# Kernel tuning notes

Hardware: AMD Instinct MI355X
Metric: run time of the kernel (lower is better)

Reference implementation:

```python
import jax, jax.numpy as jnp
import numpy as np

L_LEVELS = 10
LEVEL_DIM = 4
BASE_RES = 16
T_HASH = 2 ** 21
DEG_VIEW = 4
DENSITY_BIAS = -1.0
RGB_PADDING = 0.001
RES = (BASE_RES * 2 ** np.arange(L_LEVELS)).astype(np.float32)  # 16..8192
CORNERS = np.array([[(i >> 2) & 1, (i >> 1) & 1, i & 1] for i in range(8)], np.int32)  # [8,3]
P1 = jnp.uint32(2654435761)
P2 = jnp.uint32(805459861)


def hash_grid_encode(pts, embeddings):
    """pts [N,3] in [-1,1]; embeddings [L,T,D] -> [N,L,D] trilinear hash-grid features."""
    x01 = (pts + 1.0) * 0.5  # [N,3] in [0,1]

    def level(emb, r):
        pos = x01 * r - 0.5  # align_corners=False style
        p0 = jnp.floor(pos)
        frac = pos - p0  # [N,3]
        coords = (p0.astype(jnp.int32)[:, None, :] + CORNERS).astype(jnp.uint32)  # [N,8,3]
        h = coords[..., 0] ^ (coords[..., 1] * P1) ^ (coords[..., 2] * P2)
        idx = (h & jnp.uint32(T_HASH - 1)).astype(jnp.int32)  # [N,8]
        w = jnp.prod(jnp.where(CORNERS == 1, frac[:, None, :], 1.0 - frac[:, None, :]), axis=-1)  # [N,8]
        vals = emb[idx]  # [N,8,D]
        return jnp.einsum('ncd,nc->nd', vals, w)

    feats = jax.vmap(level)(embeddings, jnp.asarray(RES))  # [L,N,D]
    return jnp.moveaxis(feats, 0, 1)  # [N,L,D]


def pos_enc(d, min_deg=0, max_deg=DEG_VIEW):
    scales = 2.0 ** jnp.arange(min_deg, max_deg, dtype=jnp.float32)
    xb = (d[..., None, :] * scales[:, None]).reshape(*d.shape[:-1], -1)  # [...,3*deg]
    four = jnp.sin(jnp.concatenate([xb, xb + 0.5 * jnp.pi], axis=-1))
    return jnp.concatenate([d, four], axis=-1)  # [..., 3 + 6*deg] = 27


def setup_inputs() -> dict:
    key = jax.random.key(0)
    ks = jax.random.split(key, 10)
    B, S, n = 1024, 32, 6
    means = jax.random.uniform(ks[0], (B, S, n, 3), minval=-1.0, maxval=1.0)
    stds = jax.random.uniform(ks[1], (B, S, n), minval=0.001, maxval=0.05)
    vd = jax.random.normal(ks[2], (B, 3))
    viewdirs = vd / jnp.linalg.norm(vd, axis=-1, keepdims=True)
    embeddings = jax.random.normal(ks[3], (L_LEVELS, T_HASH, LEVEL_DIM)) * 0.1

    def lin(k, i, o):
        return jax.random.normal(k, (i, o)) * (1.0 / np.sqrt(i))

    return {
        'rand': 0,
        'means': means, 'stds': stds, 'viewdirs': viewdirs, 'embeddings': embeddings,
        'Wd0': lin(ks[4], 40, 64), 'bd0': jnp.zeros(64),
        'Wd1': lin(ks[5], 64, 256), 'bd1': jnp.zeros(256),
        'Wv0': lin(ks[6], 283, 256), 'bv0': jnp.zeros(256),
        'Wv1': lin(ks[7], 539, 256), 'bv1': jnp.zeros(256),
        'Wr': lin(ks[8], 256, 3), 'br': jnp.zeros(3),
    }


def reference(rand, means, stds, viewdirs, embeddings, Wd0, bd0, Wd1, bd1,
              Wv0, bv0, Wv1, bv1, Wr, br):
    B, S, n = means.shape[:3]
    # --- predict_density ---
    feats = hash_grid_encode(means.reshape(-1, 3), embeddings)
    feats = feats.reshape(B, S, n, L_LEVELS, LEVEL_DIM)
    gs = jnp.asarray(RES)
    # erf re-weighting by per-level grid size (ZipNeRF anti-aliasing)
    w = jax.lax.erf(1.0 / jnp.clip(jnp.sqrt(8.0 * stds[..., None] ** 2 * gs ** 2), 1e-10))  # [B,S,n,L]
    feat = (feats * w[..., None]).mean(axis=-3).reshape(B, S, L_LEVELS * LEVEL_DIM)  # mean over multisamples n
    h = jax.nn.relu(feat @ Wd0 + bd0)
    x = h @ Wd1 + bd1  # [B,S,256] bottleneck
    density = jax.nn.softplus(x[..., 0] + DENSITY_BIAS)
    # --- view-dependent rgb branch ---
    dir_enc = pos_enc(viewdirs)  # [B,27]
    de = jnp.broadcast_to(dir_enc[:, None, :], (B, S, dir_enc.shape[-1]))
    x_in = jnp.concatenate([x, de], axis=-1)  # [B,S,283]
    h = jax.nn.relu(x_in @ Wv0 + bv0)
    h = jnp.concatenate([h, x_in], axis=-1)  # skip connection at layer 0 -> [B,S,539]
    h = jax.nn.relu(h @ Wv1 + bv1)
    rgb = jax.nn.sigmoid(h @ Wr + br)  # rgb_premultiplier=1, rgb_bias=0
    rgb = rgb * (1.0 + 2.0 * RGB_PADDING) - RGB_PADDING
    return density, rgb
```

## Files before the change

### kernel.cpp

```cpp
#include <hip/hip_runtime.h>

#define HASH_T    2097152u
#define HASH_MASK 2097151u
#define PRIME1 2654435761u
#define PRIME2 805459861u

typedef __attribute__((ext_vector_type(8))) short bf16x8;
typedef __attribute__((ext_vector_type(4))) float f32x4;
typedef __attribute__((ext_vector_type(4))) unsigned short us4;

#define LDS_STRIDE 328

__device__ __forceinline__ unsigned short bf16_hi(float x){
    unsigned u = __float_as_uint(x);
    return (unsigned short)((u + 0x7FFFu + ((u >> 16) & 1u)) >> 16);
}
__device__ __forceinline__ float bf16f(unsigned short h){
    return __uint_as_float((unsigned)h << 16);
}
__device__ __forceinline__ void split2(float x, unsigned short& h, unsigned short& l){
    h = bf16_hi(x);
    l = bf16_hi(x - bf16f(h));
}

__global__ __launch_bounds__(256) void pack_weights_kernel(
    const float* __restrict__ Wd0, const float* __restrict__ Wd1,
    const float* __restrict__ Wv0, const float* __restrict__ Wv1,
    unsigned short* __restrict__ pk)
{
    int tid = blockIdx.x * 256 + threadIdx.x;
    if (tid >= 424 * 512) return;
    int pair = tid >> 9;
    int li   = tid & 511;
    int lane = li >> 3, j = li & 7;
    int kq = ((lane >> 4) << 3) + j;
    int cl = lane & 15;
    float w;
    if (pair < 8) {
        int idx = pair; int kt = idx >> 2, ct = idx & 3;
        int k = kt * 32 + kq, c = ct * 16 + cl;
        w = (k < 40) ? Wd0[k * 64 + c] : 0.0f;
    } else if (pair < 40) {
        int idx = pair - 8; int kt = idx >> 4, ct = idx & 15;
        int k = kt * 32 + kq, c = ct * 16 + cl;
        w = Wd1[k * 256 + c];
    } else if (pair < 168) {
        int idx = pair - 40; int kt = idx >> 4, ct = idx & 15;
        int k = kt * 32 + kq, c = ct * 16 + cl;
        w = Wv0[k * 256 + c];
    } else {
        int idx = pair - 168;
        int kt = idx >> 4, ct = idx & 15;
        int k = kt * 32 + kq, c = ct * 16 + cl;
        int refr = (k < 256) ? (k + 256) : (k - 256);
        w = Wv1[refr * 256 + c];
    }
    unsigned short h, l; split2(w, h, l);
    pk[(size_t)pair * 1024 + li]       = h;
    pk[(size_t)pair * 1024 + 512 + li] = l;
}

template<int KT, int NC>
__device__ __forceinline__ void gemm32(
    const unsigned short* __restrict__ pkBase, int NCT, int ct0, int kOff,
    const unsigned short (*Ahi)[LDS_STRIDE], const unsigned short (*Alo)[LDS_STRIDE],
    int lane, f32x4 acc[NC][2])
{
    const int r = lane & 15;
    const int kg = (lane >> 4) * 8;
    bf16x8 ah[NC], al[NC];
    #pragma unroll
    for (int ci = 0; ci < NC; ++ci) {
        const unsigned short* pf = pkBase + (size_t)(ct0 + ci) * 1024 + (size_t)lane * 8;
        ah[ci] = *reinterpret_cast<const bf16x8*>(pf);
        al[ci] = *reinterpret_cast<const bf16x8*>(pf + 512);
    }
    #pragma unroll
    for (int kt = 0; kt < KT; ++kt) {
        bf16x8 ahn[NC], aln[NC];
        if (kt + 1 < KT) {
            #pragma unroll
            for (int ci = 0; ci < NC; ++ci) {
                const unsigned short* pf = pkBase
                    + (size_t)((kt + 1) * NCT + ct0 + ci) * 1024 + (size_t)lane * 8;
                ahn[ci] = *reinterpret_cast<const bf16x8*>(pf);
                aln[ci] = *reinterpret_cast<const bf16x8*>(pf + 512);
            }
        }
        const int ke = kOff + kt * 32 + kg;
        bf16x8 bh[2], bl[2];
        #pragma unroll
        for (int st = 0; st < 2; ++st) {
            bh[st] = *reinterpret_cast<const bf16x8*>(&Ahi[st * 16 + r][ke]);
            bl[st] = *reinterpret_cast<const bf16x8*>(&Alo[st * 16 + r][ke]);
        }
        #pragma unroll
        for (int ci = 0; ci < NC; ++ci) {
            #pragma unroll
            for (int st = 0; st < 2; ++st) {
                acc[ci][st] = __builtin_amdgcn_mfma_f32_16x16x32_bf16(ah[ci], bh[st], acc[ci][st], 0, 0, 0);
                acc[ci][st] = __builtin_amdgcn_mfma_f32_16x16x32_bf16(ah[ci], bl[st], acc[ci][st], 0, 0, 0);
                acc[ci][st] = __builtin_amdgcn_mfma_f32_16x16x32_bf16(al[ci], bh[st], acc[ci][st], 0, 0, 0);
            }
        }
        if (kt + 1 < KT) {
            #pragma unroll
            for (int ci = 0; ci < NC; ++ci) { ah[ci] = ahn[ci]; al[ci] = aln[ci]; }
        }
    }
}

template<int NC, bool RELU>
__device__ __forceinline__ void epi32(
    f32x4 acc[NC][2], int ct0, int lane, const float* bias, int outOff,
    unsigned short (*Ahi)[LDS_STRIDE], unsigned short (*Alo)[LDS_STRIDE])
{
    const int r = lane & 15, g = lane >> 4;
    #pragma unroll
    for (int ci = 0; ci < NC; ++ci) {
        const int c0 = (ct0 + ci) * 16 + g * 4;
        const float4 bb = *reinterpret_cast<const float4*>(&bias[c0]);
        #pragma unroll
        for (int st = 0; st < 2; ++st) {
            const int s = st * 16 + r;
            float v[4] = { acc[ci][st][0] + bb.x, acc[ci][st][1] + bb.y,
                           acc[ci][st][2] + bb.z, acc[ci][st][3] + bb.w };
            us4 H, L;
            #pragma unroll
            for (int q = 0; q < 4; ++q) {
                float vv = RELU ? fmaxf(v[q], 0.0f) : v[q];
                unsigned short h, l; split2(vv, h, l);
                H[q] = h; L[q] = l;
            }
            *reinterpret_cast<us4*>(&Ahi[s][outOff + c0]) = H;
            *reinterpret_cast<us4*>(&Alo[s][outOff + c0]) = L;
        }
    }
}

__global__ __launch_bounds__(256, 3) void zip_fused_kernel(
    const float* __restrict__ means, const float* __restrict__ stds,
    const float* __restrict__ vdirs, const float* __restrict__ emb,
    const unsigned short* __restrict__ pk,
    const float* __restrict__ bd0, const float* __restrict__ bd1,
    const float* __restrict__ Wv0, const float* __restrict__ bv0,
    const float* __restrict__ Wv1, const float* __restrict__ bv1,
    const float* __restrict__ Wr,  const float* __restrict__ br,
    float* __restrict__ outD, float* __restrict__ outRGB)
{
    __shared__ __align__(16) unsigned short sAhi[32][LDS_STRIDE];
    __shared__ __align__(16) unsigned short sAlo[32][LDS_STRIDE];
    __shared__ float sDe[32];
    __shared__ float sDv0[256];
    __shared__ float sDv1[256];

    const int t = threadIdx.x;
    const int lane = t & 63;
    const int w = t >> 6;
    const int b = blockIdx.x;
    const int base = b * 32;

    if (t < 192) {
        int s = t / 6, j = t - s * 6;
        us4 z = {0, 0, 0, 0};
        *reinterpret_cast<us4*>(&sAhi[s][40 + j * 4]) = z;
        *reinterpret_cast<us4*>(&sAlo[s][40 + j * 4]) = z;
    }
    if (t < 27) {
        float d0 = vdirs[b * 3 + 0], d1 = vdirs[b * 3 + 1], d2 = vdirs[b * 3 + 2];
        float val;
        if (t < 3) val = (t == 0) ? d0 : ((t == 1) ? d1 : d2);
        else {
            int u = t - 3, half = u / 12, jk = u % 12;
            int j = jk / 3, k = jk % 3;
            float dk = (k == 0) ? d0 : ((k == 1) ? d1 : d2);
            float xb = dk * (float)(1 << j);
            val = sinf(half ? (xb + 1.57079632679489662f) : xb);
        }
        sDe[t] = val;
    }
    __syncthreads();

    {
        const int s = t >> 3, n = t & 7;
        const bool act = (n < 6);
        float mx = 0.f, my = 0.f, mz = 0.f, sd2_8 = 0.f;
        if (act) {
            const float* mp = means + ((size_t)(base + s) * 6 + n) * 3;
            mx = mp[0]; my = mp[1]; mz = mp[2];
            float sd = stds[(size_t)(base + s) * 6 + n];
            sd2_8 = 8.0f * sd * sd;
        }
        const float inv6 = 1.0f / 6.0f;
        #pragma unroll 2
        for (int l = 0; l < 10; ++l) {
            float r = (float)(16 << l);
            float a0 = 0.f, a1 = 0.f, a2 = 0.f, a3 = 0.f;
            if (act) {
                float px = (mx + 1.0f) * 0.5f * r - 0.5f;
                float py = (my + 1.0f) * 0.5f * r - 0.5f;
                float pz = (mz + 1.0f) * 0.5f * r - 0.5f;
                float fx = floorf(px), fy = floorf(py), fz = floorf(pz);
                float rx = px - fx, ry = py - fy, rz = pz - fz;
                int ix = (int)fx, iy = (int)fy, iz = (int)fz;
                unsigned hx[2] = { (unsigned)ix,          (unsigned)(ix + 1) };
                unsigned hy[2] = { (unsigned)iy * PRIME1, (unsigned)(iy + 1) * PRIME1 };
                unsigned hz[2] = { (unsigned)iz * PRIME2, (unsigned)(iz + 1) * PRIME2 };
                float wx[2] = { 1.0f - rx, rx };
                float wy[2] = { 1.0f - ry, ry };
                float wz[2] = { 1.0f - rz, rz };
                float wl = erff(1.0f / fmaxf(sqrtf(sd2_8 * r * r), 1e-10f));
                #pragma unroll
                for (int c = 0; c < 8; ++c) {
                    int cx = (c >> 2) & 1, cy = (c >> 1) & 1, cz = c & 1;
                    unsigned idx = (hx[cx] ^ hy[cy] ^ hz[cz]) & HASH_MASK;
                    const float4 e = *reinterpret_cast<const float4*>(
                        emb + ((size_t)l * HASH_T + idx) * 4u);
                    float wgt = wx[cx] * wy[cy] * wz[cz];
                    a0 += wgt * e.x; a1 += wgt * e.y; a2 += wgt * e.z; a3 += wgt * e.w;
                }
                a0 *= wl; a1 *= wl; a2 *= wl; a3 *= wl;
            }
            #pragma unroll
            for (int m = 1; m < 8; m <<= 1) {
                a0 += __shfl_xor(a0, m);
                a1 += __shfl_xor(a1, m);
                a2 += __shfl_xor(a2, m);
                a3 += __shfl_xor(a3, m);
            }
            if (n == 0) {
                float o[4] = { a0 * inv6, a1 * inv6, a2 * inv6, a3 * inv6 };
                us4 H, L;
                #pragma unroll
                for (int q = 0; q < 4; ++q) {
                    unsigned short h, lo; split2(o[q], h, lo);
                    H[q] = h; L[q] = lo;
                }
                *reinterpret_cast<us4*>(&sAhi[s][l * 4]) = H;
                *reinterpret_cast<us4*>(&sAlo[s][l * 4]) = L;
            }
        }
    }
    __syncthreads();

    {
        int c = t;
        float a0 = bv0[c], a1 = bv1[c];
        #pragma unroll 3
        for (int k = 0; k < 27; ++k) {
            float dv = sDe[k];
            a0 += dv * Wv0[(256 + k) * 256 + c];
            a1 += dv * Wv1[(512 + k) * 256 + c];
        }
        sDv0[c] = a0; sDv1[c] = a1;
    }
    __syncthreads();

    {
        f32x4 acc[1][2] = {};
        gemm32<2, 1>(pk, 4, w, 0, sAhi, sAlo, lane, acc);
        __syncthreads();
        epi32<1, true>(acc, w, lane, bd0, 0, sAhi, sAlo);
    }
    __syncthreads();

    {
        f32x4 acc[4][2] = {};
        gemm32<2, 4>(pk + 8192, 16, w * 4, 0, sAhi, sAlo, lane, acc);
        if (w == 0 && (lane >> 4) == 0) {
            #pragma unroll
            for (int st = 0; st < 2; ++st) {
                float x0 = acc[0][st][0] + bd1[0];
                int s = st * 16 + (lane & 15);
                float vv = x0 - 1.0f;
                outD[base + s] = fmaxf(vv, 0.0f) + log1pf(expf(-fabsf(vv)));
            }
        }
        __syncthreads();
        epi32<4, false>(acc, w * 4, lane, bd1, 64, sAhi, sAlo);
    }
    __syncthreads();

    f32x4 px[4][2] = {};
    gemm32<8, 4>(pk + 172032, 16, w * 4, 64, sAhi, sAlo, lane, px);
    __syncthreads();

    {
        f32x4 acc[4][2] = {};
        gemm32<8, 4>(pk + 40960, 16, w * 4, 64, sAhi, sAlo, lane, acc);
        __syncthreads();
        epi32<4, true>(acc, w * 4, lane, sDv0, 64, sAhi, sAlo);
    }
    __syncthreads();

    {
        gemm32<8, 4>(pk + 303104, 16, w * 4, 64, sAhi, sAlo, lane, px);
        __syncthreads();
        epi32<4, true>(px, w * 4, lane, sDv1, 64, sAhi, sAlo);
    }
    __syncthreads();

    {
        int s = t >> 3, j = t & 7, k0 = 64 + j * 32;
        float p0 = 0.f, p1 = 0.f, p2 = 0.f;
        #pragma unroll 2
        for (int q = 0; q < 4; ++q) {
            us4 vh[2], vl[2];
            *reinterpret_cast<uint4*>(vh) = *reinterpret_cast<const uint4*>(&sAhi[s][k0 + q * 8]);
            *reinterpret_cast<uint4*>(vl) = *reinterpret_cast<const uint4*>(&sAlo[s][k0 + q * 8]);
            #pragma unroll
            for (int e = 0; e < 8; ++e) {
                int k = j * 32 + q * 8 + e;
                float hv = bf16f(((const unsigned short*)vh)[e]) + bf16f(((const unsigned short*)vl)[e]);
                p0 += hv * Wr[k * 3 + 0];
                p1 += hv * Wr[k * 3 + 1];
                p2 += hv * Wr[k * 3 + 2];
            }
        }
        #pragma unroll
        for (int m = 1; m < 8; m <<= 1) {
            p0 += __shfl_xor(p0, m);
            p1 += __shfl_xor(p1, m);
            p2 += __shfl_xor(p2, m);
        }
        if (j < 3) {
            float a = ((j == 0) ? p0 : (j == 1) ? p1 : p2) + br[j];
            float sg = 1.0f / (1.0f + expf(-a));
            outRGB[(size_t)(base + s) * 3 + j] = sg * 1.002f - 0.001f;
        }
    }
}

extern "C" void kernel_launch(void* const* d_in, const int* in_sizes, int n_in,
                              void* d_out, int out_size, void* d_ws, size_t ws_size,
                              hipStream_t stream) {
    const float* means = (const float*)d_in[1];
    const float* stds_ = (const float*)d_in[2];
    const float* vdirs = (const float*)d_in[3];
    const float* emb   = (const float*)d_in[4];
    const float* Wd0 = (const float*)d_in[5];
    const float* bd0 = (const float*)d_in[6];
    const float* Wd1 = (const float*)d_in[7];
    const float* bd1 = (const float*)d_in[8];
    const float* Wv0 = (const float*)d_in[9];
    const float* bv0 = (const float*)d_in[10];
    const float* Wv1 = (const float*)d_in[11];
    const float* bv1 = (const float*)d_in[12];
    const float* Wr  = (const float*)d_in[13];
    const float* br  = (const float*)d_in[14];

    const int B  = in_sizes[3] / 3;
    const int NS = B * 32;

    unsigned short* pk = (unsigned short*)d_ws;

    hipLaunchKernelGGL(pack_weights_kernel, dim3((424 * 512 + 255) / 256), dim3(256), 0, stream,
                       Wd0, Wd1, Wv0, Wv1, pk);

    float* outD   = (float*)d_out;
    float* outRGB = outD + NS;
    hipLaunchKernelGGL(zip_fused_kernel, dim3(B), dim3(256), 0, stream,
                       means, stds_, vdirs, emb, pk,
                       bd0, bd1, Wv0, bv0, Wv1, bv1, Wr, br,
                       outD, outRGB);
}
```

Measured before the change: 191.4 us.

## Keep density-branch activations in single bf16 and shrink LDS to raise occupancy

The hash-grid features and the first density hidden layer are now stored as plain bf16 in a separate 32x64 LDS buffer, not as hi/lo bf16 pairs. The two density GEMMs use a new two-MFMA routine that drops the low-activation term. The bottleneck and view-branch activations keep hi/lo in smaller 264-wide buffers, which cuts LDS per block, and launch bounds are raised from 3 to 4 blocks per CU. The trade is lower precision in the density MLP inputs and some register pressure from the new bound.

After: 216.4 us. +13.1%, slower.

```diff
diff --git a/kernel.cpp b/kernel.cpp
--- a/kernel.cpp
+++ b/kernel.cpp
@@ -9,7 +9,7 @@
 typedef __attribute__((ext_vector_type(4))) float f32x4;
 typedef __attribute__((ext_vector_type(4))) unsigned short us4;
 
-#define LDS_STRIDE 328
+#define XS 264
 
 __device__ __forceinline__ unsigned short bf16_hi(float x){
     unsigned u = __float_as_uint(x);
@@ -62,8 +62,8 @@
 
 template<int KT, int NC>
 __device__ __forceinline__ void gemm32(
-    const unsigned short* __restrict__ pkBase, int NCT, int ct0, int kOff,
-    const unsigned short (*Ahi)[LDS_STRIDE], const unsigned short (*Alo)[LDS_STRIDE],
+    const unsigned short* __restrict__ pkBase, int NCT, int ct0,
+    const unsigned short (*Bhi)[XS], const unsigned short (*Blo)[XS],
     int lane, f32x4 acc[NC][2])
 {
     const int r = lane & 15;
@@ -87,12 +87,12 @@
                 aln[ci] = *reinterpret_cast<const bf16x8*>(pf + 512);
             }
         }
-        const int ke = kOff + kt * 32 + kg;
+        const int ke = kt * 32 + kg;
         bf16x8 bh[2], bl[2];
         #pragma unroll
         for (int st = 0; st < 2; ++st) {
-            bh[st] = *reinterpret_cast<const bf16x8*>(&Ahi[st * 16 + r][ke]);
-            bl[st] = *reinterpret_cast<const bf16x8*>(&Alo[st * 16 + r][ke]);
+            bh[st] = *reinterpret_cast<const bf16x8*>(&Bhi[st * 16 + r][ke]);
+            bl[st] = *reinterpret_cast<const bf16x8*>(&Blo[st * 16 + r][ke]);
         }
         #pragma unroll
         for (int ci = 0; ci < NC; ++ci) {
@@ -110,10 +110,56 @@
     }
 }
 
+template<int KT, int NC>
+__device__ __forceinline__ void gemm_sf(
+    const unsigned short* __restrict__ pkBase, int NCT, int ct0,
+    const unsigned short (*B)[64], int lane, f32x4 acc[NC][2])
+{
+    const int r = lane & 15;
+    const int kg = (lane >> 4) * 8;
+    bf16x8 ah[NC], al[NC];
+    #pragma unroll
+    for (int ci = 0; ci < NC; ++ci) {
+        const unsigned short* pf = pkBase + (size_t)(ct0 + ci) * 1024 + (size_t)lane * 8;
+        ah[ci] = *reinterpret_cast<const bf16x8*>(pf);
+        al[ci] = *reinterpret_cast<const bf16x8*>(pf + 512);
+    }
+    #pragma unroll
+    for (int kt = 0; kt < KT; ++kt) {
+        bf16x8 ahn[NC], aln[NC];
+        if (kt + 1 < KT) {
+            #pragma unroll
+            for (int ci = 0; ci < NC; ++ci) {
+                const unsigned short* pf = pkBase
+                    + (size_t)((kt + 1) * NCT + ct0 + ci) * 1024 + (size_t)lane * 8;
+                ahn[ci] = *reinterpret_cast<const bf16x8*>(pf);
+                aln[ci] = *reinterpret_cast<const bf16x8*>(pf + 512);
+            }
+        }
+        const int ke = kt * 32 + kg;
+        bf16x8 bh[2];
+        #pragma unroll
+        for (int st = 0; st < 2; ++st)
+            bh[st] = *reinterpret_cast<const bf16x8*>(&B[st * 16 + r][ke]);
+        #pragma unroll
+        for (int ci = 0; ci < NC; ++ci) {
+            #pragma unroll
+            for (int st = 0; st < 2; ++st) {
+                acc[ci][st] = __builtin_amdgcn_mfma_f32_16x16x32_bf16(ah[ci], bh[st], acc[ci][st], 0, 0, 0);
+                acc[ci][st] = __builtin_amdgcn_mfma_f32_16x16x32_bf16(al[ci], bh[st], acc[ci][st], 0, 0, 0);
+            }
+        }
+        if (kt + 1 < KT) {
+            #pragma unroll
+            for (int ci = 0; ci < NC; ++ci) { ah[ci] = ahn[ci]; al[ci] = aln[ci]; }
+        }
+    }
+}
+
 template<int NC, bool RELU>
 __device__ __forceinline__ void epi32(
-    f32x4 acc[NC][2], int ct0, int lane, const float* bias, int outOff,
-    unsigned short (*Ahi)[LDS_STRIDE], unsigned short (*Alo)[LDS_STRIDE])
+    f32x4 acc[NC][2], int ct0, int lane, const float* bias,
+    unsigned short (*Bhi)[XS], unsigned short (*Blo)[XS])
 {
     const int r = lane & 15, g = lane >> 4;
     #pragma unroll
@@ -132,13 +178,13 @@
                 unsigned short h, l; split2(vv, h, l);
                 H[q] = h; L[q] = l;
             }
-            *reinterpret_cast<us4*>(&Ahi[s][outOff + c0]) = H;
-            *reinterpret_cast<us4*>(&Alo[s][outOff + c0]) = L;
-        }
-    }
-}
-
-__global__ __launch_bounds__(256, 3) void zip_fused_kernel(
+            *reinterpret_cast<us4*>(&Bhi[s][c0]) = H;
+            *reinterpret_cast<us4*>(&Blo[s][c0]) = L;
+        }
+    }
+}
+
+__global__ __launch_bounds__(256, 4) void zip_fused_kernel(
     const float* __restrict__ means, const float* __restrict__ stds,
     const float* __restrict__ vdirs, const float* __restrict__ emb,
     const unsigned short* __restrict__ pk,
@@ -148,8 +194,9 @@
     const float* __restrict__ Wr,  const float* __restrict__ br,
     float* __restrict__ outD, float* __restrict__ outRGB)
 {
-    __shared__ __align__(16) unsigned short sAhi[32][LDS_STRIDE];
-    __shared__ __align__(16) unsigned short sAlo[32][LDS_STRIDE];
+    __shared__ __align__(16) unsigned short sF[32][64];
+    __shared__ __align__(16) unsigned short sXhi[32][XS];
+    __shared__ __align__(16) unsigned short sXlo[32][XS];
     __shared__ float sDe[32];
     __shared__ float sDv0[256];
     __shared__ float sDv1[256];
@@ -163,8 +210,7 @@
     if (t < 192) {
         int s = t / 6, j = t - s * 6;
         us4 z = {0, 0, 0, 0};
-        *reinterpret_cast<us4*>(&sAhi[s][40 + j * 4]) = z;
-        *reinterpret_cast<us4*>(&sAlo[s][40 + j * 4]) = z;
+        *reinterpret_cast<us4*>(&sF[s][40 + j * 4]) = z;
     }
     if (t < 27) {
         float d0 = vdirs[b * 3 + 0], d1 = vdirs[b * 3 + 1], d2 = vdirs[b * 3 + 2];
@@ -229,15 +275,12 @@
                 a3 += __shfl_xor(a3, m);
             }
             if (n == 0) {
-                float o[4] = { a0 * inv6, a1 * inv6, a2 * inv6, a3 * inv6 };
-                us4 H, L;
-                #pragma unroll
-                for (int q = 0; q < 4; ++q) {
-                    unsigned short h, lo; split2(o[q], h, lo);
-                    H[q] = h; L[q] = lo;
-                }
-                *reinterpret_cast<us4*>(&sAhi[s][l * 4]) = H;
-                *reinterpret_cast<us4*>(&sAlo[s][l * 4]) = L;
+                us4 H;
+                H[0] = bf16_hi(a0 * inv6);
+                H[1] = bf16_hi(a1 * inv6);
+                H[2] = bf16_hi(a2 * inv6);
+                H[3] = bf16_hi(a3 * inv6);
+                *reinterpret_cast<us4*>(&sF[s][l * 4]) = H;
             }
         }
     }
@@ -258,15 +301,27 @@
 
     {
         f32x4 acc[1][2] = {};
-        gemm32<2, 1>(pk, 4, w, 0, sAhi, sAlo, lane, acc);
+        gemm_sf<2, 1>(pk, 4, w, sF, lane, acc);
         __syncthreads();
-        epi32<1, true>(acc, w, lane, bd0, 0, sAhi, sAlo);
+        const int r = lane & 15, g = lane >> 4;
+        const int c0 = w * 16 + g * 4;
+        const float4 bb = *reinterpret_cast<const float4*>(&bd0[c0]);
+        #pragma unroll
+        for (int st = 0; st < 2; ++st) {
+            const int s = st * 16 + r;
+            us4 H;
+            H[0] = bf16_hi(fmaxf(acc[0][st][0] + bb.x, 0.0f));
+            H[1] = bf16_hi(fmaxf(acc[0][st][1] + bb.y, 0.0f));
+            H[2] = bf16_hi(fmaxf(acc[0][st][2] + bb.z, 0.0f));
+            H[3] = bf16_hi(fmaxf(acc[0][st][3] + bb.w, 0.0f));
+            *reinterpret_cast<us4*>(&sF[s][c0]) = H;
+        }
     }
     __syncthreads();
 
     {
         f32x4 acc[4][2] = {};
-        gemm32<2, 4>(pk + 8192, 16, w * 4, 0, sAhi, sAlo, lane, acc);
+        gemm_sf<2, 4>(pk + 8192, 16, w * 4, sF, lane, acc);
         if (w == 0 && (lane >> 4) == 0) {
             #pragma unroll
             for (int st = 0; st < 2; ++st) {
@@ -276,41 +331,40 @@
                 outD[base + s] = fmaxf(vv, 0.0f) + log1pf(expf(-fabsf(vv)));
             }
         }
+        epi32<4, false>(acc, w * 4, lane, bd1, sXhi, sXlo);
+    }
+    __syncthreads();
+
+    f32x4 px[4][2] = {};
+    gemm32<8, 4>(pk + 172032, 16, w * 4, sXhi, sXlo, lane, px);
+    __syncthreads();
+
+    {
+        f32x4 acc[4][2] = {};
+        gemm32<8, 4>(pk + 40960, 16, w * 4, sXhi, sXlo, lane, acc);
         __syncthreads();
-        epi32<4, false>(acc, w * 4, lane, bd1, 64, sAhi, sAlo);
-    }
-    __syncthreads();
-
-    f32x4 px[4][2] = {};
-    gemm32<8, 4>(pk + 172032, 16, w * 4, 64, sAhi, sAlo, lane, px);
-    __syncthreads();
-
-    {
-        f32x4 acc[4][2] = {};
-        gemm32<8, 4>(pk + 40960, 16, w * 4, 64, sAhi, sAlo, lane, acc);
+        epi32<4, true>(acc, w * 4, lane, sDv0, sXhi, sXlo);
+    }
+    __syncthreads();
+
+    {
+        gemm32<8, 4>(pk + 303104, 16, w * 4, sXhi, sXlo, lane, px);
         __syncthreads();
-        epi32<4, true>(acc, w * 4, lane, sDv0, 64, sAhi, sAlo);
-    }
-    __syncthreads();
-
-    {
-        gemm32<8, 4>(pk + 303104, 16, w * 4, 64, sAhi, sAlo, lane, px);
-        __syncthreads();
-        epi32<4, true>(px, w * 4, lane, sDv1, 64, sAhi, sAlo);
-    }
-    __syncthreads();
-
-    {
-        int s = t >> 3, j = t & 7, k0 = 64 + j * 32;
+        epi32<4, true>(px, w * 4, lane, sDv1, sXhi, sXlo);
+    }
+    __syncthreads();
+
+    {
+        int s = t >> 3, j = t & 7, k0 = j * 32;
         float p0 = 0.f, p1 = 0.f, p2 = 0.f;
         #pragma unroll 2
         for (int q = 0; q < 4; ++q) {
             us4 vh[2], vl[2];
-            *reinterpret_cast<uint4*>(vh) = *reinterpret_cast<const uint4*>(&sAhi[s][k0 + q * 8]);
-            *reinterpret_cast<uint4*>(vl) = *reinterpret_cast<const uint4*>(&sAlo[s][k0 + q * 8]);
+            *reinterpret_cast<uint4*>(vh) = *reinterpret_cast<const uint4*>(&sXhi[s][k0 + q * 8]);
+            *reinterpret_cast<uint4*>(vl) = *reinterpret_cast<const uint4*>(&sXlo[s][k0 + q * 8]);
             #pragma unroll
             for (int e = 0; e < 8; ++e) {
-                int k = j * 32 + q * 8 + e;
+                int k = k0 + q * 8 + e;
                 float hv = bf16f(((const unsigned short*)vh)[e]) + bf16f(((const unsigned short*)vl)[e]);
                 p0 += hv * Wr[k * 3 + 0];
                 p1 += hv * Wr[k * 3 + 1];
```

## Halve samples per block and spread hash-grid corners across threads

Applied to the files above, without the earlier changes.

Each block now handles 16 samples instead of 32, which doubles the grid size and halves LDS use per block. The MFMA GEMMs shrink to a single 16-row tile. The hash-grid encode changes its thread mapping: each thread owns one corner for three multisamples instead of all eight corners for one sample. It processes two levels per iteration to issue more independent gathers, then reduces across 16 lanes. The aim is more memory-level parallelism and occupancy for the random embedding gathers, at the cost of loading the weight fragments twice as often per sample and recomputing the view-direction encoding per block.

After: 189.4 us. No clear change (-1.1%).

```diff
diff --git a/kernel.cpp b/kernel.cpp
--- a/kernel.cpp
+++ b/kernel.cpp
@@ -61,10 +61,10 @@
 }
 
 template<int KT, int NC>
-__device__ __forceinline__ void gemm32(
+__device__ __forceinline__ void gemm16(
     const unsigned short* __restrict__ pkBase, int NCT, int ct0, int kOff,
     const unsigned short (*Ahi)[LDS_STRIDE], const unsigned short (*Alo)[LDS_STRIDE],
-    int lane, f32x4 acc[NC][2])
+    int lane, f32x4 acc[NC])
 {
     const int r = lane & 15;
     const int kg = (lane >> 4) * 8;
@@ -88,20 +88,13 @@
             }
         }
         const int ke = kOff + kt * 32 + kg;
-        bf16x8 bh[2], bl[2];
-        #pragma unroll
-        for (int st = 0; st < 2; ++st) {
-            bh[st] = *reinterpret_cast<const bf16x8*>(&Ahi[st * 16 + r][ke]);
-            bl[st] = *reinterpret_cast<const bf16x8*>(&Alo[st * 16 + r][ke]);
-        }
+        bf16x8 bh = *reinterpret_cast<const bf16x8*>(&Ahi[r][ke]);
+        bf16x8 bl = *reinterpret_cast<const bf16x8*>(&Alo[r][ke]);
         #pragma unroll
         for (int ci = 0; ci < NC; ++ci) {
-            #pragma unroll
-            for (int st = 0; st < 2; ++st) {
-                acc[ci][st] = __builtin_amdgcn_mfma_f32_16x16x32_bf16(ah[ci], bh[st], acc[ci][st], 0, 0, 0);
-                acc[ci][st] = __builtin_amdgcn_mfma_f32_16x16x32_bf16(ah[ci], bl[st], acc[ci][st], 0, 0, 0);
-                acc[ci][st] = __builtin_amdgcn_mfma_f32_16x16x32_bf16(al[ci], bh[st], acc[ci][st], 0, 0, 0);
-            }
+            acc[ci] = __builtin_amdgcn_mfma_f32_16x16x32_bf16(ah[ci], bh, acc[ci], 0, 0, 0);
+            acc[ci] = __builtin_amdgcn_mfma_f32_16x16x32_bf16(ah[ci], bl, acc[ci], 0, 0, 0);
+            acc[ci] = __builtin_amdgcn_mfma_f32_16x16x32_bf16(al[ci], bh, acc[ci], 0, 0, 0);
         }
         if (kt + 1 < KT) {
             #pragma unroll
@@ -111,8 +104,8 @@
 }
 
 template<int NC, bool RELU>
-__device__ __forceinline__ void epi32(
-    f32x4 acc[NC][2], int ct0, int lane, const float* bias, int outOff,
+__device__ __forceinline__ void epi16(
+    f32x4 acc[NC], int ct0, int lane, const float* bias, int outOff,
     unsigned short (*Ahi)[LDS_STRIDE], unsigned short (*Alo)[LDS_STRIDE])
 {
     const int r = lane & 15, g = lane >> 4;
@@ -120,21 +113,17 @@
     for (int ci = 0; ci < NC; ++ci) {
         const int c0 = (ct0 + ci) * 16 + g * 4;
         const float4 bb = *reinterpret_cast<const float4*>(&bias[c0]);
+        float v[4] = { acc[ci][0] + bb.x, acc[ci][1] + bb.y,
+                       acc[ci][2] + bb.z, acc[ci][3] + bb.w };
+        us4 H, L;
         #pragma unroll
-        for (int st = 0; st < 2; ++st) {
-            const int s = st * 16 + r;
-            float v[4] = { acc[ci][st][0] + bb.x, acc[ci][st][1] + bb.y,
-                           acc[ci][st][2] + bb.z, acc[ci][st][3] + bb.w };
-            us4 H, L;
-            #pragma unroll
-            for (int q = 0; q < 4; ++q) {
-                float vv = RELU ? fmaxf(v[q], 0.0f) : v[q];
-                unsigned short h, l; split2(vv, h, l);
-                H[q] = h; L[q] = l;
-            }
-            *reinterpret_cast<us4*>(&Ahi[s][outOff + c0]) = H;
-            *reinterpret_cast<us4*>(&Alo[s][outOff + c0]) = L;
-        }
+        for (int q = 0; q < 4; ++q) {
+            float vv = RELU ? fmaxf(v[q], 0.0f) : v[q];
+            unsigned short h, l; split2(vv, h, l);
+            H[q] = h; L[q] = l;
+        }
+        *reinterpret_cast<us4*>(&Ahi[r][outOff + c0]) = H;
+        *reinterpret_cast<us4*>(&Alo[r][outOff + c0]) = L;
     }
 }
 
@@ -148,8 +137,8 @@
     const float* __restrict__ Wr,  const float* __restrict__ br,
     float* __restrict__ outD, float* __restrict__ outRGB)
 {
-    __shared__ __align__(16) unsigned short sAhi[32][LDS_STRIDE];
-    __shared__ __align__(16) unsigned short sAlo[32][LDS_STRIDE];
+    __shared__ __align__(16) unsigned short sAhi[16][LDS_STRIDE];
+    __shared__ __align__(16) unsigned short sAlo[16][LDS_STRIDE];
     __shared__ float sDe[32];
     __shared__ float sDv0[256];
     __shared__ float sDv1[256];
@@ -158,16 +147,17 @@
     const int lane = t & 63;
     const int w = t >> 6;
     const int b = blockIdx.x;
-    const int base = b * 32;
-
-    if (t < 192) {
+    const int ray = b >> 1;
+    const int base = b * 16;
+
+    if (t < 96) {
         int s = t / 6, j = t - s * 6;
         us4 z = {0, 0, 0, 0};
         *reinterpret_cast<us4*>(&sAhi[s][40 + j * 4]) = z;
         *reinterpret_cast<us4*>(&sAlo[s][40 + j * 4]) = z;
     }
     if (t < 27) {
-        float d0 = vdirs[b * 3 + 0], d1 = vdirs[b * 3 + 1], d2 = vdirs[b * 3 + 2];
+        float d0 = vdirs[ray * 3 + 0], d1 = vdirs[ray * 3 + 1], d2 = vdirs[ray * 3 + 2];
         float val;
         if (t < 3) val = (t == 0) ? d0 : ((t == 1) ? d1 : d2);
         else {
@@ -182,62 +172,72 @@
     __syncthreads();
 
     {
-        const int s = t >> 3, n = t & 7;
-        const bool act = (n < 6);
-        float mx = 0.f, my = 0.f, mz = 0.f, sd2_8 = 0.f;
-        if (act) {
+        const int s = t >> 4, u = t & 15;
+        const int c = u >> 1, h = u & 1;
+        const int cxb = (c >> 2) & 1, cyb = (c >> 1) & 1, czb = c & 1;
+        float mx[3], my[3], mz[3], s28[3];
+        #pragma unroll
+        for (int q = 0; q < 3; ++q) {
+            int n = h * 3 + q;
             const float* mp = means + ((size_t)(base + s) * 6 + n) * 3;
-            mx = mp[0]; my = mp[1]; mz = mp[2];
+            mx[q] = mp[0]; my[q] = mp[1]; mz[q] = mp[2];
             float sd = stds[(size_t)(base + s) * 6 + n];
-            sd2_8 = 8.0f * sd * sd;
+            s28[q] = 8.0f * sd * sd;
         }
         const float inv6 = 1.0f / 6.0f;
-        #pragma unroll 2
-        for (int l = 0; l < 10; ++l) {
-            float r = (float)(16 << l);
-            float a0 = 0.f, a1 = 0.f, a2 = 0.f, a3 = 0.f;
-            if (act) {
-                float px = (mx + 1.0f) * 0.5f * r - 0.5f;
-                float py = (my + 1.0f) * 0.5f * r - 0.5f;
-                float pz = (mz + 1.0f) * 0.5f * r - 0.5f;
-                float fx = floorf(px), fy = floorf(py), fz = floorf(pz);
-                float rx = px - fx, ry = py - fy, rz = pz - fz;
-                int ix = (int)fx, iy = (int)fy, iz = (int)fz;
-                unsigned hx[2] = { (unsigned)ix,          (unsigned)(ix + 1) };
-                unsigned hy[2] = { (unsigned)iy * PRIME1, (unsigned)(iy + 1) * PRIME1 };
-                unsigned hz[2] = { (unsigned)iz * PRIME2, (unsigned)(iz + 1) * PRIME2 };
-                float wx[2] = { 1.0f - rx, rx };
-                float wy[2] = { 1.0f - ry, ry };
-                float wz[2] = { 1.0f - rz, rz };
-                float wl = erff(1.0f / fmaxf(sqrtf(sd2_8 * r * r), 1e-10f));
+        #pragma unroll 1
+        for (int lp = 0; lp < 5; ++lp) {
+            float4 ev[2][3];
+            float cw[2][3];
+            #pragma unroll
+            for (int dl = 0; dl < 2; ++dl) {
+                const int l = lp * 2 + dl;
+                const float r = (float)(16 << l);
+                const float* embL = emb + (size_t)l * HASH_T * 4u;
                 #pragma unroll
-                for (int c = 0; c < 8; ++c) {
-                    int cx = (c >> 2) & 1, cy = (c >> 1) & 1, cz = c & 1;
-                    unsigned idx = (hx[cx] ^ hy[cy] ^ hz[cz]) & HASH_MASK;
-                    const float4 e = *reinterpret_cast<const float4*>(
-                        emb + ((size_t)l * HASH_T + idx) * 4u);
-                    float wgt = wx[cx] * wy[cy] * wz[cz];
-                    a0 += wgt * e.x; a1 += wgt * e.y; a2 += wgt * e.z; a3 += wgt * e.w;
+                for (int q = 0; q < 3; ++q) {
+                    float px = (mx[q] + 1.0f) * 0.5f * r - 0.5f;
+                    float py = (my[q] + 1.0f) * 0.5f * r - 0.5f;
+                    float pz = (mz[q] + 1.0f) * 0.5f * r - 0.5f;
+                    float fx = floorf(px), fy = floorf(py), fz = floorf(pz);
+                    float rx = px - fx, ry = py - fy, rz = pz - fz;
+                    unsigned hx = (unsigned)((int)fx + cxb);
+                    unsigned hy = (unsigned)((int)fy + cyb) * PRIME1;
+                    unsigned hz = (unsigned)((int)fz + czb) * PRIME2;
+                    unsigned idx = (hx ^ hy ^ hz) & HASH_MASK;
+                    float wx = cxb ? rx : 1.0f - rx;
+                    float wy = cyb ? ry : 1.0f - ry;
+                    float wz = czb ? rz : 1.0f - rz;
+                    float wl = erff(1.0f / fmaxf(sqrtf(s28[q] * r * r), 1e-10f));
+                    cw[dl][q] = wx * wy * wz * wl;
+                    ev[dl][q] = *reinterpret_cast<const float4*>(embL + (size_t)idx * 4u);
                 }
-                a0 *= wl; a1 *= wl; a2 *= wl; a3 *= wl;
             }
             #pragma unroll
-            for (int m = 1; m < 8; m <<= 1) {
-                a0 += __shfl_xor(a0, m);
-                a1 += __shfl_xor(a1, m);
-                a2 += __shfl_xor(a2, m);
-                a3 += __shfl_xor(a3, m);
-            }
-            if (n == 0) {
-                float o[4] = { a0 * inv6, a1 * inv6, a2 * inv6, a3 * inv6 };
-                us4 H, L;
+            for (int dl = 0; dl < 2; ++dl) {
+                float a0 = cw[dl][0]*ev[dl][0].x + cw[dl][1]*ev[dl][1].x + cw[dl][2]*ev[dl][2].x;
+                float a1 = cw[dl][0]*ev[dl][0].y + cw[dl][1]*ev[dl][1].y + cw[dl][2]*ev[dl][2].y;
+                float a2 = cw[dl][0]*ev[dl][0].z + cw[dl][1]*ev[dl][1].z + cw[dl][2]*ev[dl][2].z;
+                float a3 = cw[dl][0]*ev[dl][0].w + cw[dl][1]*ev[dl][1].w + cw[dl][2]*ev[dl][2].w;
                 #pragma unroll
-                for (int q = 0; q < 4; ++q) {
-                    unsigned short h, lo; split2(o[q], h, lo);
-                    H[q] = h; L[q] = lo;
+                for (int m = 1; m < 16; m <<= 1) {
+                    a0 += __shfl_xor(a0, m);
+                    a1 += __shfl_xor(a1, m);
+                    a2 += __shfl_xor(a2, m);
+                    a3 += __shfl_xor(a3, m);
                 }
-                *reinterpret_cast<us4*>(&sAhi[s][l * 4]) = H;
-                *reinterpret_cast<us4*>(&sAlo[s][l * 4]) = L;
+                if (u == 0) {
+                    const int l = lp * 2 + dl;
+                    float o[4] = { a0 * inv6, a1 * inv6, a2 * inv6, a3 * inv6 };
+                    us4 H, L;
+                    #pragma unroll
+                    for (int q = 0; q < 4; ++q) {
+                        unsigned short hh, ll; split2(o[q], hh, ll);
+                        H[q] = hh; L[q] = ll;
+                    }
+                    *reinterpret_cast<us4*>(&sAhi[s][l * 4]) = H;
+                    *reinterpret_cast<us4*>(&sAlo[s][l * 4]) = L;
+                }
             }
         }
     }
@@ -257,50 +257,46 @@
     __syncthreads();
 
     {
-        f32x4 acc[1][2] = {};
-        gemm32<2, 1>(pk, 4, w, 0, sAhi, sAlo, lane, acc);
+        f32x4 acc[1] = {};
+        gemm16<2, 1>(pk, 4, w, 0, sAhi, sAlo, lane, acc);
         __syncthreads();
-        epi32<1, true>(acc, w, lane, bd0, 0, sAhi, sAlo);
-    }
-    __syncthreads();
-
-    {
-        f32x4 acc[4][2] = {};
-        gemm32<2, 4>(pk + 8192, 16, w * 4, 0, sAhi, sAlo, lane, acc);
-        if (w == 0 && (lane >> 4) == 0) {
-            #pragma unroll
-            for (int st = 0; st < 2; ++st) {
-                float x0 = acc[0][st][0] + bd1[0];
-                int s = st * 16 + (lane & 15);
-                float vv = x0 - 1.0f;
-                outD[base + s] = fmaxf(vv, 0.0f) + log1pf(expf(-fabsf(vv)));
-            }
+        epi16<1, true>(acc, w, lane, bd0, 0, sAhi, sAlo);
+    }
+    __syncthreads();
+
+    {
+        f32x4 acc[4] = {};
+        gemm16<2, 4>(pk + 8192, 16, w * 4, 0, sAhi, sAlo, lane, acc);
+        if (w == 0 && lane < 16) {
+            float x0 = acc[0][0] + bd1[0];
+            float vv = x0 - 1.0f;
+            outD[base + lane] = fmaxf(vv, 0.0f) + log1pf(expf(-fabsf(vv)));
         }
         __syncthreads();
-        epi32<4, false>(acc, w * 4, lane, bd1, 64, sAhi, sAlo);
-    }
-    __syncthreads();
-
-    f32x4 px[4][2] = {};
-    gemm32<8, 4>(pk + 172032, 16, w * 4, 64, sAhi, sAlo, lane, px);
-    __syncthreads();
-
-    {
-        f32x4 acc[4][2] = {};
-        gemm32<8, 4>(pk + 40960, 16, w * 4, 64, sAhi, sAlo, lane, acc);
+        epi16<4, false>(acc, w * 4, lane, bd1, 64, sAhi, sAlo);
+    }
+    __syncthreads();
+
+    f32x4 px[4] = {};
+    gemm16<8, 4>(pk + 172032, 16, w * 4, 64, sAhi, sAlo, lane, px);
+    __syncthreads();
+
+    {
+        f32x4 acc[4] = {};
+        gemm16<8, 4>(pk + 40960, 16, w * 4, 64, sAhi, sAlo, lane, acc);
         __syncthreads();
-        epi32<4, true>(acc, w * 4, lane, sDv0, 64, sAhi, sAlo);
-    }
-    __syncthreads();
-
-    {
-        gemm32<8, 4>(pk + 303104, 16, w * 4, 64, sAhi, sAlo, lane, px);
+        epi16<4, true>(acc, w * 4, lane, sDv0, 64, sAhi, sAlo);
+    }
+    __syncthreads();
+
+    {
+        gemm16<8, 4>(pk + 303104, 16, w * 4, 64, sAhi, sAlo, lane, px);
         __syncthreads();
-        epi32<4, true>(px, w * 4, lane, sDv1, 64, sAhi, sAlo);
-    }
-    __syncthreads();
-
-    {
+        epi16<4, true>(px, w * 4, lane, sDv1, 64, sAhi, sAlo);
+    }
+    __syncthreads();
+
+    if (t < 128) {
         int s = t >> 3, j = t & 7, k0 = 64 + j * 32;
         float p0 = 0.f, p1 = 0.f, p2 = 0.f;
         #pragma unroll 2
@@ -359,7 +355,7 @@
 
     float* outD   = (float*)d_out;
     float* outRGB = outD + NS;
-    hipLaunchKernelGGL(zip_fused_kernel, dim3(B), dim3(256), 0, stream,
+    hipLaunchKernelGGL(zip_fused_kernel, dim3(NS / 16), dim3(256), 0, stream,
                        means, stds_, vdirs, emb, pk,
                        bd0, bd1, Wv0, bv0, Wv1, bv1, Wr, br,
                        outD, outRGB);
```
